# Kernel tuning notes

Hardware: AMD Instinct MI355X
Metric: run time of the kernel (lower is better)

## Reference

```python
import jax, jax.numpy as jnp
import numpy as np

N_NODES = 163842
SEQ_LEN = 9
IN_CH = 32
OUT_CH = 64


def setup_inputs() -> dict:
    key = jax.random.key(0)
    k1, k2, k3 = jax.random.split(key, 3)
    x = jax.random.normal(k1, (N_NODES, IN_CH), dtype=jnp.float32)
    indices = jax.random.randint(k2, (N_NODES, SEQ_LEN), 0, N_NODES, dtype=jnp.int64)
    # xavier_uniform for Linear(IN_CH*SEQ_LEN, OUT_CH)
    fan_in = IN_CH * SEQ_LEN
    limit = float(np.sqrt(6.0 / (fan_in + OUT_CH)))
    W = jax.random.uniform(k3, (OUT_CH, fan_in), dtype=jnp.float32, minval=-limit, maxval=limit)
    b = jnp.zeros((OUT_CH,), dtype=jnp.float32)
    return {"x": x, "indices": indices, "W": W, "b": b}


def reference(x, indices, W, b):
    # gather spiral neighbor features: [n_nodes, seq_len, in_ch]
    gathered = x[indices]
    # flatten to [n_nodes, seq_len*in_ch] and apply Linear (y = g @ W^T + b)
    g = gathered.reshape(indices.shape[0], -1)
    return jnp.einsum("nf,of->no", g, W) + b
```

## Files before the change

### kernel.cpp

```cpp
#include <hip/hip_runtime.h>
#include <hip/hip_bf16.h>


constexpr int NN   = 163842;
constexpr int SEQ  = 9;
constexpr int INC  = 32;
constexpr int OUTC = 64;
constexpr int FAN  = SEQ * INC;

using s8    = __attribute__((ext_vector_type(8))) short;
using f32x4 = __attribute__((ext_vector_type(4))) float;

__device__ __forceinline__ unsigned f2bf(float f) {
    union { float f; unsigned u; } c; c.f = f;
    unsigned u = c.u;
    u += 0x7fffu + ((u >> 16) & 1u);
    return (u >> 16) & 0xffffu;
}

__global__ __launch_bounds__(256) void convert_bf16_kernel(
    const float* __restrict__ x, const float* __restrict__ W,
    unsigned short* __restrict__ xb, unsigned short* __restrict__ wb)
{
    const int xq = NN * INC / 4;
    const int wq = OUTC * FAN / 4;
    int i = blockIdx.x * blockDim.x + threadIdx.x;
    if (i < xq) {
        float4 v = reinterpret_cast<const float4*>(x)[i];
        unsigned lo = f2bf(v.x) | (f2bf(v.y) << 16);
        unsigned hi = f2bf(v.z) | (f2bf(v.w) << 16);
        reinterpret_cast<uint2*>(xb)[i] = make_uint2(lo, hi);
    } else if (i < xq + wq) {
        int j = i - xq;
        float4 v = reinterpret_cast<const float4*>(W)[j];
        unsigned lo = f2bf(v.x) | (f2bf(v.y) << 16);
        unsigned hi = f2bf(v.z) | (f2bf(v.w) << 16);
        reinterpret_cast<uint2*>(wb)[j] = make_uint2(lo, hi);
    }
}

__global__ __launch_bounds__(256) void spiral_gemm_kernel(
    const int* __restrict__ idx,
    const unsigned short* __restrict__ xb,
    const unsigned short* __restrict__ wb,
    const float* __restrict__ bias,
    float* __restrict__ out)
{
    const int lane = threadIdx.x & 63;
    const int wid  = threadIdx.x >> 6;
    const int lc   = lane & 15;
    const int lk   = lane >> 4;
    const int kb   = lk * 8;

    const int nodeBase = blockIdx.x * 128 + wid * 32;

    const int r0 = min(nodeBase + lc,      NN - 1);
    const int r1 = min(nodeBase + 16 + lc, NN - 1);

    int n0[SEQ], n1[SEQ];
    #pragma unroll
    for (int s = 0; s < SEQ; ++s) {
        n0[s] = idx[r0 * SEQ + s];
        n1[s] = idx[r1 * SEQ + s];
    }
    s8 xf0[SEQ], xf1[SEQ];
    #pragma unroll
    for (int s = 0; s < SEQ; ++s) {
        xf0[s] = *reinterpret_cast<const s8*>(xb + (size_t)n0[s] * INC + kb);
        xf1[s] = *reinterpret_cast<const s8*>(xb + (size_t)n1[s] * INC + kb);
    }

    f32x4 acc[2][4] = {};
    #pragma unroll
    for (int s = 0; s < SEQ; ++s) {
        #pragma unroll
        for (int f = 0; f < 4; ++f) {
            s8 wfrag = *reinterpret_cast<const s8*>(wb + (f * 16 + lc) * FAN + s * 32 + kb);
            acc[0][f] = __builtin_amdgcn_mfma_f32_16x16x32_bf16(wfrag, xf0[s], acc[0][f], 0, 0, 0);
            acc[1][f] = __builtin_amdgcn_mfma_f32_16x16x32_bf16(wfrag, xf1[s], acc[1][f], 0, 0, 0);
        }
    }

    #pragma unroll
    for (int f = 0; f < 4; ++f) {
        const float4 b4 = *reinterpret_cast<const float4*>(bias + f * 16 + lk * 4);
        #pragma unroll
        for (int m = 0; m < 2; ++m) {
            const int node = nodeBase + m * 16 + lc;
            if (node < NN) {
                float4 v;
                v.x = acc[m][f][0] + b4.x;
                v.y = acc[m][f][1] + b4.y;
                v.z = acc[m][f][2] + b4.z;
                v.w = acc[m][f][3] + b4.w;
                *reinterpret_cast<float4*>(out + (size_t)node * OUTC + f * 16 + lk * 4) = v;
            }
        }
    }
}

extern "C" void kernel_launch(void* const* d_in, const int* in_sizes, int n_in,
                              void* d_out, int out_size, void* d_ws, size_t ws_size,
                              hipStream_t stream) {
    const float* x    = (const float*)d_in[0];
    const int*   idx  = (const int*)d_in[1];
    const float* W    = (const float*)d_in[2];
    const float* b    = (const float*)d_in[3];
    float*       out  = (float*)d_out;

    unsigned short* xb = (unsigned short*)d_ws;
    unsigned short* wb = xb + (size_t)NN * INC;

    const int totalq = (NN * INC + OUTC * FAN) / 4;
    convert_bf16_kernel<<<(totalq + 255) / 256, 256, 0, stream>>>(x, W, xb, wb);

    const int nblocks = (NN + 127) / 128;
    spiral_gemm_kernel<<<nblocks, 256, 0, stream>>>(idx, xb, wb, b, out);
}
```

Before: 47.26 us.

## Stage weights and spiral indices in LDS with swizzled layout

```diff
diff --git a/kernel.cpp b/kernel.cpp
--- a/kernel.cpp
+++ b/kernel.cpp
@@ -7,6 +7,7 @@
 constexpr int INC  = 32;
 constexpr int OUTC = 64;
 constexpr int FAN  = SEQ * INC;
+constexpr int IDX_TOT = NN * SEQ;
 
 using s8    = __attribute__((ext_vector_type(8))) short;
 using f32x4 = __attribute__((ext_vector_type(4))) float;
@@ -46,22 +47,41 @@
     const float* __restrict__ bias,
     float* __restrict__ out)
 {
-    const int lane = threadIdx.x & 63;
-    const int wid  = threadIdx.x >> 6;
+    __shared__ unsigned char wlds[64 * 576];
+    __shared__ int ilds[128 * SEQ];
+
+    const int tid  = threadIdx.x;
+    const int lane = tid & 63;
+    const int wid  = tid >> 6;
     const int lc   = lane & 15;
     const int lk   = lane >> 4;
     const int kb   = lk * 8;
 
-    const int nodeBase = blockIdx.x * 128 + wid * 32;
+    const int blockNode = blockIdx.x * 128;
 
-    const int r0 = min(nodeBase + lc,      NN - 1);
-    const int r1 = min(nodeBase + 16 + lc, NN - 1);
+    {
+        const int base = blockNode * SEQ;
+        #pragma unroll
+        for (int k = 0; k < 5; ++k) {
+            int i = tid + k * 256;
+            if (i < 128 * SEQ) {
+                int g = base + i;
+                if (g > IDX_TOT - 1) g = IDX_TOT - 1;
+                ilds[i] = idx[g];
+            }
+        }
+    }
+    __syncthreads();
 
+    const int nl0 = wid * 32 + lc;
+    const int nl1 = nl0 + 16;
     int n0[SEQ], n1[SEQ];
     #pragma unroll
     for (int s = 0; s < SEQ; ++s) {
-        n0[s] = idx[r0 * SEQ + s];
-        n1[s] = idx[r1 * SEQ + s];
+        unsigned a = (unsigned)ilds[nl0 * SEQ + s];
+        unsigned b = (unsigned)ilds[nl1 * SEQ + s];
+        n0[s] = (a >= (unsigned)NN) ? 0 : (int)a;
+        n1[s] = (b >= (unsigned)NN) ? 0 : (int)b;
     }
     s8 xf0[SEQ], xf1[SEQ];
     #pragma unroll
@@ -70,30 +90,41 @@
         xf1[s] = *reinterpret_cast<const s8*>(xb + (size_t)n1[s] * INC + kb);
     }
 
+    {
+        const uint4* w4 = reinterpret_cast<const uint4*>(wb);
+        #pragma unroll
+        for (int k = 0; k < 9; ++k) {
+            int i4  = tid + k * 256;
+            int row = i4 / 36;
+            int c16 = i4 % 36;
+            unsigned boff = (unsigned)(row * 576 + c16 * 16) ^ ((unsigned)(row & 7) << 4);
+            *reinterpret_cast<uint4*>(&wlds[boff]) = w4[i4];
+        }
+    }
+    __syncthreads();
+
     f32x4 acc[2][4] = {};
     #pragma unroll
     for (int s = 0; s < SEQ; ++s) {
         #pragma unroll
         for (int f = 0; f < 4; ++f) {
-            s8 wfrag = *reinterpret_cast<const s8*>(wb + (f * 16 + lc) * FAN + s * 32 + kb);
-            acc[0][f] = __builtin_amdgcn_mfma_f32_16x16x32_bf16(wfrag, xf0[s], acc[0][f], 0, 0, 0);
-            acc[1][f] = __builtin_amdgcn_mfma_f32_16x16x32_bf16(wfrag, xf1[s], acc[1][f], 0, 0, 0);
+            const int row = f * 16 + lc;
+            unsigned boff = (unsigned)(row * 576 + s * 64 + lk * 16) ^ ((unsigned)(lc & 7) << 4);
+            s8 wf = *reinterpret_cast<const s8*>(&wlds[boff]);
+            acc[0][f] = __builtin_amdgcn_mfma_f32_16x16x32_bf16(wf, xf0[s], acc[0][f], 0, 0, 0);
+            acc[1][f] = __builtin_amdgcn_mfma_f32_16x16x32_bf16(wf, xf1[s], acc[1][f], 0, 0, 0);
         }
     }
 
     #pragma unroll
     for (int f = 0; f < 4; ++f) {
-        const float4 b4 = *reinterpret_cast<const float4*>(bias + f * 16 + lk * 4);
+        const f32x4 b4 = *reinterpret_cast<const f32x4*>(bias + f * 16 + lk * 4);
         #pragma unroll
         for (int m = 0; m < 2; ++m) {
-            const int node = nodeBase + m * 16 + lc;
+            const int node = blockNode + wid * 32 + m * 16 + lc;
             if (node < NN) {
-                float4 v;
-                v.x = acc[m][f][0] + b4.x;
-                v.y = acc[m][f][1] + b4.y;
-                v.z = acc[m][f][2] + b4.z;
-                v.w = acc[m][f][3] + b4.w;
-                *reinterpret_cast<float4*>(out + (size_t)node * OUTC + f * 16 + lk * 4) = v;
+                f32x4 v = acc[m][f] + b4;
+                *reinterpret_cast<f32x4*>(out + (size_t)node * OUTC + f * 16 + lk * 4) = v;
             }
         }
     }
```

Measured after the change: 48.22 us. 1.02x slower.

## Repack x into k-chunk planes and stage padded W in LDS for MFMA

Applied to the files above, without the earlier changes.

```diff
diff --git a/kernel.cpp b/kernel.cpp
--- a/kernel.cpp
+++ b/kernel.cpp
@@ -7,6 +7,11 @@
 constexpr int INC  = 32;
 constexpr int OUTC = 64;
 constexpr int FAN  = SEQ * INC;
+constexpr int NKA  = 4;
+constexpr int KC   = 8;
+constexpr int SPAD = 12;
+constexpr int SROW = 64 * 16 + 64;
+constexpr int WTOT = NKA * SPAD * OUTC * KC;
 
 using s8    = __attribute__((ext_vector_type(8))) short;
 using f32x4 = __attribute__((ext_vector_type(4))) float;
@@ -18,82 +23,111 @@
     return (u >> 16) & 0xffffu;
 }
 
-__global__ __launch_bounds__(256) void convert_bf16_kernel(
+__global__ __launch_bounds__(256) void convert_pack_kernel(
     const float* __restrict__ x, const float* __restrict__ W,
-    unsigned short* __restrict__ xb, unsigned short* __restrict__ wb)
+    unsigned short* __restrict__ xk,
+    unsigned short* __restrict__ wk)
 {
-    const int xq = NN * INC / 4;
-    const int wq = OUTC * FAN / 4;
-    int i = blockIdx.x * blockDim.x + threadIdx.x;
-    if (i < xq) {
-        float4 v = reinterpret_cast<const float4*>(x)[i];
-        unsigned lo = f2bf(v.x) | (f2bf(v.y) << 16);
-        unsigned hi = f2bf(v.z) | (f2bf(v.w) << 16);
-        reinterpret_cast<uint2*>(xb)[i] = make_uint2(lo, hi);
-    } else if (i < xq + wq) {
-        int j = i - xq;
-        float4 v = reinterpret_cast<const float4*>(W)[j];
-        unsigned lo = f2bf(v.x) | (f2bf(v.y) << 16);
-        unsigned hi = f2bf(v.z) | (f2bf(v.w) << 16);
-        reinterpret_cast<uint2*>(wb)[j] = make_uint2(lo, hi);
+    const int t   = blockIdx.x * blockDim.x + threadIdx.x;
+    const int xq2 = NN * 2;
+    if (t < xq2) {
+        const int n = t >> 1, h = t & 1;
+        const float4* px = reinterpret_cast<const float4*>(x + (size_t)n * INC + h * 16);
+        float4 a = px[0], b = px[1], c = px[2], d = px[3];
+        uint4 lo, hi;
+        lo.x = f2bf(a.x) | (f2bf(a.y) << 16);
+        lo.y = f2bf(a.z) | (f2bf(a.w) << 16);
+        lo.z = f2bf(b.x) | (f2bf(b.y) << 16);
+        lo.w = f2bf(b.z) | (f2bf(b.w) << 16);
+        hi.x = f2bf(c.x) | (f2bf(c.y) << 16);
+        hi.y = f2bf(c.z) | (f2bf(c.w) << 16);
+        hi.z = f2bf(d.x) | (f2bf(d.y) << 16);
+        hi.w = f2bf(d.z) | (f2bf(d.w) << 16);
+        reinterpret_cast<uint4*>(xk)[(size_t)(2 * h)     * NN + n] = lo;
+        reinterpret_cast<uint4*>(xk)[(size_t)(2 * h + 1) * NN + n] = hi;
+    } else if (t < xq2 + WTOT) {
+        const int j  = t - xq2;
+        const int c  = j & 7;
+        const int o  = (j >> 3) & 63;
+        const int r  = j >> 9;
+        const int s  = r % SPAD;
+        const int ka = r / SPAD;
+        float v = (s < SEQ) ? W[(size_t)o * FAN + s * INC + ka * KC + c] : 0.0f;
+        wk[j] = (unsigned short)f2bf(v);
     }
 }
 
 __global__ __launch_bounds__(256) void spiral_gemm_kernel(
     const int* __restrict__ idx,
-    const unsigned short* __restrict__ xb,
-    const unsigned short* __restrict__ wb,
+    const unsigned short* __restrict__ xk,
+    const unsigned short* __restrict__ wk,
     const float* __restrict__ bias,
     float* __restrict__ out)
 {
-    const int lane = threadIdx.x & 63;
-    const int wid  = threadIdx.x >> 6;
+    __shared__ unsigned char wlds[NKA * SPAD * SROW];
+
+    const int tid  = threadIdx.x;
+    const int lane = tid & 63;
+    const int wid  = tid >> 6;
     const int lc   = lane & 15;
     const int lk   = lane >> 4;
-    const int kb   = lk * 8;
+
+    {
+        const uint4* w4 = reinterpret_cast<const uint4*>(wk);
+        #pragma unroll
+        for (int k = 0; k < 12; ++k) {
+            int i4   = tid + k * 256;
+            int ka   = i4 / (SPAD * 64);
+            int r    = i4 - ka * (SPAD * 64);
+            int s    = r >> 6, o = r & 63;
+            *reinterpret_cast<uint4*>(&wlds[(ka * SPAD + s) * SROW + o * 16]) = w4[i4];
+        }
+    }
 
     const int nodeBase = blockIdx.x * 128 + wid * 32;
-
-    const int r0 = min(nodeBase + lc,      NN - 1);
-    const int r1 = min(nodeBase + 16 + lc, NN - 1);
-
-    int n0[SEQ], n1[SEQ];
+    const int nd0 = min(nodeBase + lc,      NN - 1);
+    const int nd1 = min(nodeBase + 16 + lc, NN - 1);
+    int iv0[3], iv1[3];
     #pragma unroll
-    for (int s = 0; s < SEQ; ++s) {
-        n0[s] = idx[r0 * SEQ + s];
-        n1[s] = idx[r1 * SEQ + s];
+    for (int g = 0; g < 3; ++g) {
+        int s = g * 4 + lk; if (s > 8) s = 8;
+        iv0[g] = idx[(size_t)nd0 * SEQ + s];
+        iv1[g] = idx[(size_t)nd1 * SEQ + s];
     }
-    s8 xf0[SEQ], xf1[SEQ];
-    #pragma unroll
-    for (int s = 0; s < SEQ; ++s) {
-        xf0[s] = *reinterpret_cast<const s8*>(xb + (size_t)n0[s] * INC + kb);
-        xf1[s] = *reinterpret_cast<const s8*>(xb + (size_t)n1[s] * INC + kb);
-    }
+    __syncthreads();
 
     f32x4 acc[2][4] = {};
     #pragma unroll
-    for (int s = 0; s < SEQ; ++s) {
+    for (int ka = 0; ka < NKA; ++ka) {
+        const unsigned short* xa = xk + (size_t)ka * NN * KC;
+        s8 b0[3], b1[3];
         #pragma unroll
-        for (int f = 0; f < 4; ++f) {
-            s8 wfrag = *reinterpret_cast<const s8*>(wb + (f * 16 + lc) * FAN + s * 32 + kb);
-            acc[0][f] = __builtin_amdgcn_mfma_f32_16x16x32_bf16(wfrag, xf0[s], acc[0][f], 0, 0, 0);
-            acc[1][f] = __builtin_amdgcn_mfma_f32_16x16x32_bf16(wfrag, xf1[s], acc[1][f], 0, 0, 0);
+        for (int g = 0; g < 3; ++g) {
+            b0[g] = *reinterpret_cast<const s8*>(xa + (size_t)iv0[g] * KC);
+            b1[g] = *reinterpret_cast<const s8*>(xa + (size_t)iv1[g] * KC);
+        }
+        #pragma unroll
+        for (int g = 0; g < 3; ++g) {
+            #pragma unroll
+            for (int f = 0; f < 4; ++f) {
+                const int s = g * 4 + lk;
+                s8 wf = *reinterpret_cast<const s8*>(
+                    &wlds[(ka * SPAD + s) * SROW + (f * 16 + lc) * 16]);
+                acc[0][f] = __builtin_amdgcn_mfma_f32_16x16x32_bf16(wf, b0[g], acc[0][f], 0, 0, 0);
+                acc[1][f] = __builtin_amdgcn_mfma_f32_16x16x32_bf16(wf, b1[g], acc[1][f], 0, 0, 0);
+            }
         }
     }
 
     #pragma unroll
     for (int f = 0; f < 4; ++f) {
-        const float4 b4 = *reinterpret_cast<const float4*>(bias + f * 16 + lk * 4);
+        const f32x4 b4 = *reinterpret_cast<const f32x4*>(bias + f * 16 + lk * 4);
         #pragma unroll
         for (int m = 0; m < 2; ++m) {
             const int node = nodeBase + m * 16 + lc;
             if (node < NN) {
-                float4 v;
-                v.x = acc[m][f][0] + b4.x;
-                v.y = acc[m][f][1] + b4.y;
-                v.z = acc[m][f][2] + b4.z;
-                v.w = acc[m][f][3] + b4.w;
-                *reinterpret_cast<float4*>(out + (size_t)node * OUTC + f * 16 + lk * 4) = v;
+                f32x4 v = acc[m][f] + b4;
+                *reinterpret_cast<f32x4*>(out + (size_t)node * OUTC + f * 16 + lk * 4) = v;
             }
         }
     }
@@ -108,12 +142,12 @@
     const float* b    = (const float*)d_in[3];
     float*       out  = (float*)d_out;
 
-    unsigned short* xb = (unsigned short*)d_ws;
-    unsigned short* wb = xb + (size_t)NN * INC;
+    unsigned short* xk = (unsigned short*)d_ws;
+    unsigned short* wk = xk + (size_t)NKA * NN * KC;
 
-    const int totalq = (NN * INC + OUTC * FAN) / 4;
-    convert_bf16_kernel<<<(totalq + 255) / 256, 256, 0, stream>>>(x, W, xb, wb);
+    const int ctot = NN * 2 + WTOT;
+    convert_pack_kernel<<<(ctot + 255) / 256, 256, 0, stream>>>(x, W, xk, wk);
 
     const int nblocks = (NN + 127) / 128;
-    spiral_gemm_kernel<<<nblocks, 256, 0, stream>>>(idx, xb, wb, b, out);
+    spiral_gemm_kernel<<<nblocks, 256, 0, stream>>>(idx, xk, wk, b, out);
 }
```

Measured after the change: 61.97 us. 31.1% more time.
